# Kernel optimization log

Measured on AMD Instinct MI355X. Metric: run time of the kernel, lower is better.

The kernel has to match this reference:

```python
import jax, jax.numpy as jnp
import numpy as np

E = 1024   # embed_dim
H = 16     # num_heads
D = E // H # head_dim = 64
Q = 4      # num_queries
B = 4
S = 2048


def setup_inputs() -> dict:
    key = jax.random.key(0)
    ks = jax.random.split(key, 9)
    s = 0.02  # init scale for weights
    return {
        "x":  jax.random.normal(ks[0], (B, S, E), jnp.float32),
        "Wq": jax.random.normal(ks[1], (Q, E, E), jnp.float32) * s,  # stacked per-query Linear weights (torch layout: out,in)
        "bq": jax.random.normal(ks[2], (Q, E), jnp.float32) * s,
        "Wk": jax.random.normal(ks[3], (E, E), jnp.float32) * s,
        "bk": jax.random.normal(ks[4], (E,), jnp.float32) * s,
        "Wv": jax.random.normal(ks[5], (E, E), jnp.float32) * s,
        "bv": jax.random.normal(ks[6], (E,), jnp.float32) * s,
        "Wo": jax.random.normal(ks[7], (E, E), jnp.float32) * s,
        "bo": jax.random.normal(ks[8], (E,), jnp.float32) * s,
    }


def reference(x, Wq, bq, Wk, bk, Wv, bv, Wo, bo):
    B_, S_, E_ = x.shape
    scale = 1.0 / jnp.sqrt(jnp.asarray(D, x.dtype))
    # all query projections at once: (Q,B,S,E) -> (Q,B,S,H,D)
    q = (jnp.einsum('bse,qfe->qbsf', x, Wq) + bq[:, None, None, :]).reshape(Q, B_, S_, H, D)
    k = (x @ Wk.T + bk).reshape(B_, S_, H, D)
    v = (x @ Wv.T + bv).reshape(B_, S_, H, D)
    # NOTE: faithful to the torch code, which never moves the head axis before matmul:
    # scores[q,b,s,h,g] = sum_d q[q,b,s,h,d] * k[b,s,g,d]  -> softmax over heads g
    scores = jnp.einsum('qbshd,bsgd->qbshg', q, k) * scale      # (Q,B,S,H,H)
    probs = jax.nn.softmax(scores, axis=-1)
    out = jnp.einsum('qbshg,bsgd->qbshd', probs, v)             # (Q,B,S,H,D)
    # torch: .transpose(1,2).contiguous().view(B,S,E) == permute to (B,H,S,D) then reshape
    out = jnp.transpose(out, (0, 1, 3, 2, 4)).reshape(Q, B_, S_, E_)
    out = out.sum(axis=0)
    return out @ Wo.T + bo
```

## Files before the change

kernel.cpp:

```cpp
#include <hip/hip_runtime.h>


typedef __bf16 bf16x8 __attribute__((ext_vector_type(8)));
typedef float f32x4 __attribute__((ext_vector_type(4)));
typedef float f32x16 __attribute__((ext_vector_type(16)));

__device__ __forceinline__ unsigned short f2b(float f) {
  unsigned u = __float_as_uint(f);
  return (unsigned short)((u + 0x7fffu + ((u >> 16) & 1u)) >> 16);
}

__device__ __forceinline__ void async16(const void* g, void* l) {
  __builtin_amdgcn_global_load_lds(
      (const __attribute__((address_space(1))) void*)g,
      (__attribute__((address_space(3))) void*)l, 16, 0, 0);
}

__global__ __launch_bounds__(256) void cvt_all(
    const float* __restrict__ x, const float* __restrict__ Wq, const float* __restrict__ Wk,
    const float* __restrict__ Wv, const float* __restrict__ Wo, const float* __restrict__ bq,
    const float* __restrict__ bk, const float* __restrict__ bv,
    unsigned short* __restrict__ xb, unsigned short* __restrict__ wcat,
    unsigned short* __restrict__ wo_b, float* __restrict__ biascat) {
  if (blockIdx.x >= 15360) {
    int j = (blockIdx.x - 15360) * 256 + threadIdx.x;
    if (j < 6144) {
      float v = (j < 4096) ? bq[j] : (j < 5120 ? bk[j - 4096] : bv[j - 5120]);
      biascat[j] = v;
    }
    return;
  }
  int i = blockIdx.x * 256 + threadIdx.x;
  const float* s;
  unsigned short* d;
  int off;
  if (i < 2097152)      { s = x;  d = xb;             off = i; }
  else if (i < 3145728) { s = Wq; d = wcat;           off = i - 2097152; }
  else if (i < 3407872) { s = Wk; d = wcat + 4194304; off = i - 3145728; }
  else if (i < 3670016) { s = Wv; d = wcat + 5242880; off = i - 3407872; }
  else                  { s = Wo; d = wo_b;           off = i - 3670016; }
  float4 v = ((const float4*)s)[off];
  uint2 o;
  o.x = (unsigned)f2b(v.x) | ((unsigned)f2b(v.y) << 16);
  o.y = (unsigned)f2b(v.z) | ((unsigned)f2b(v.w) << 16);
  ((uint2*)d)[off] = o;
}

__global__ __launch_bounds__(512, 2) void gemm256(
    const unsigned short* __restrict__ A, const unsigned short* __restrict__ Bt,
    const float* __restrict__ bias, unsigned short* __restrict__ C,
    int M, int N, int K) {
  __shared__ __align__(16) unsigned short As[4][8192];
  __shared__ __align__(16) unsigned short Bs[4][8192];
  const int t = threadIdx.x;
  const int lane = t & 63, w = t >> 6;
  const int l31 = lane & 31, lhi = lane >> 5;
  const int wm = (w >> 2) * 128, wn = (w & 3) * 64;
  const int bm0 = blockIdx.y * 256, bn0 = blockIdx.x * 256;

  const int p0 = t & 7, pr0 = t >> 3;
  const int u0 = p0 ^ (pr0 & 7);
  const size_t aoff0 = (size_t)(2 * pr0 + (u0 & 1)) * K + (u0 >> 1) * 8;
  const unsigned short* aS0 = A + (size_t)bm0 * K + aoff0;
  const unsigned short* aS1 = aS0 + (size_t)128 * K;
  const unsigned short* bS0 = Bt + (size_t)bn0 * K + aoff0;
  const unsigned short* bS1 = bS0 + (size_t)128 * K;
  const int d0 = t * 8, d1 = d0 + 4096;

  const int plo = 2 * lhi + (l31 & 1);
  const int pswz = (l31 >> 1) & 7;
  const int pg0 = ((0 + plo) ^ pswz) * 8;
  const int pg1 = ((4 + plo) ^ pswz) * 8;
  int prA[4], prB[2];
#pragma unroll
  for (int mi = 0; mi < 4; ++mi) prA[mi] = ((wm + mi * 32 + l31) >> 1) * 64;
#pragma unroll
  for (int nj = 0; nj < 2; ++nj) prB[nj] = ((wn + nj * 32 + l31) >> 1) * 64;

  f32x16 acc[4][2];
#pragma unroll
  for (int mi = 0; mi < 4; ++mi)
#pragma unroll
    for (int nj = 0; nj < 2; ++nj)
#pragma unroll
      for (int e = 0; e < 16; ++e) acc[mi][nj][e] = 0.f;

#define STG_A(kt_) do { const int b_ = (kt_) & 3; const int ko_ = (kt_) * 32; \
    async16(aS0 + ko_, &As[b_][d0]); async16(aS1 + ko_, &As[b_][d1]); } while (0)
#define STG_B(kt_) do { const int b_ = (kt_) & 3; const int ko_ = (kt_) * 32; \
    async16(bS0 + ko_, &Bs[b_][d0]); async16(bS1 + ko_, &Bs[b_][d1]); } while (0)

  const int NT = K >> 5;
  STG_A(0); STG_B(0); STG_A(1); STG_B(1);
  asm volatile("s_waitcnt vmcnt(4)" ::: "memory");
  asm volatile("s_barrier" ::: "memory");

  for (int kt = 0; kt < NT; ++kt) {
    const int bi = kt & 3;
    const unsigned short* as_ = As[bi];
    const unsigned short* bs_ = Bs[bi];

    bf16x8 af[4][2], bfv[2][2];
#pragma unroll
    for (int mi = 0; mi < 4; ++mi) {
      af[mi][0] = *(const bf16x8*)(as_ + prA[mi] + pg0);
      af[mi][1] = *(const bf16x8*)(as_ + prA[mi] + pg1);
    }
#pragma unroll
    for (int nj = 0; nj < 2; ++nj) {
      bfv[nj][0] = *(const bf16x8*)(bs_ + prB[nj] + pg0);
      bfv[nj][1] = *(const bf16x8*)(bs_ + prB[nj] + pg1);
    }
    if (kt + 2 < NT) { STG_A(kt + 2); STG_B(kt + 2); }

#pragma unroll
    for (int mi = 0; mi < 4; ++mi)
#pragma unroll
      for (int nj = 0; nj < 2; ++nj) {
        acc[mi][nj] = __builtin_amdgcn_mfma_f32_32x32x16_bf16(af[mi][0], bfv[nj][0], acc[mi][nj], 0, 0, 0);
        acc[mi][nj] = __builtin_amdgcn_mfma_f32_32x32x16_bf16(af[mi][1], bfv[nj][1], acc[mi][nj], 0, 0, 0);
      }

    if (kt + 2 < NT) {
      asm volatile("s_waitcnt vmcnt(4)" ::: "memory");
    } else if (kt + 1 < NT) {
      asm volatile("s_waitcnt vmcnt(0)" ::: "memory");
    }
    asm volatile("s_barrier" ::: "memory");
  }
#undef STG_A
#undef STG_B

#pragma unroll
  for (int mi = 0; mi < 4; ++mi) {
#pragma unroll
    for (int nj = 0; nj < 2; ++nj) {
      int gc = bn0 + wn + nj * 32 + l31;
      float bsv = bias[gc];
#pragma unroll
      for (int reg = 0; reg < 16; ++reg) {
        int gr = bm0 + wm + mi * 32 + (reg & 3) + 8 * (reg >> 2) + 4 * lhi;
        C[(size_t)gr * N + gc] = f2b(acc[mi][nj][reg] + bsv);
      }
    }
  }
}

template <typename OutT>
__global__ __launch_bounds__(256) void gemm_bt(const unsigned short* __restrict__ A,
                                               const unsigned short* __restrict__ Bt,
                                               const float* __restrict__ bias,
                                               OutT* __restrict__ C, int M, int N, int K) {
  __shared__ __align__(16) unsigned short As[128 * 64];
  __shared__ __align__(16) unsigned short Bs[128 * 64];
  const int t = threadIdx.x;
  const int lane = t & 63, w = t >> 6;
  const int wm = (w >> 1) * 64, wn = (w & 1) * 64;
  const int l31 = lane & 31, lhi = lane >> 5;
  const int bm0 = blockIdx.y * 128, bn0 = blockIdx.x * 128;

  f32x16 acc[2][2];
#pragma unroll
  for (int i = 0; i < 2; ++i)
#pragma unroll
    for (int j = 0; j < 2; ++j)
#pragma unroll
      for (int e = 0; e < 16; ++e) acc[i][j][e] = 0.f;

  const int swz = l31 & 7;
  const int qoff = 2 * ((l31 >> 4) & 1);

  for (int k0 = 0; k0 < K; k0 += 64) {
    __syncthreads();
#pragma unroll
    for (int j = 0; j < 4; ++j) {
      int slot = j * 256 + t;
      int r = slot >> 3;
      int p = slot & 7;
      int c = (((p ^ (r & 7)) - 2 * ((r >> 4) & 1)) & 7) * 8;
      async16(A + (size_t)(bm0 + r) * K + k0 + c, As + slot * 8);
      async16(Bt + (size_t)(bn0 + r) * K + k0 + c, Bs + slot * 8);
    }
    __syncthreads();
#pragma unroll
    for (int kk = 0; kk < 64; kk += 16) {
      const int kg = kk >> 3;
      const int pg = ((((kg + lhi + qoff) & 7) ^ swz) << 3);
      bf16x8 af[2], bfr[2];
#pragma unroll
      for (int i = 0; i < 2; ++i)
        af[i] = *(const bf16x8*)(As + (wm + i * 32 + l31) * 64 + pg);
#pragma unroll
      for (int j = 0; j < 2; ++j)
        bfr[j] = *(const bf16x8*)(Bs + (wn + j * 32 + l31) * 64 + pg);
#pragma unroll
      for (int i = 0; i < 2; ++i)
#pragma unroll
        for (int j = 0; j < 2; ++j)
          acc[i][j] = __builtin_amdgcn_mfma_f32_32x32x16_bf16(af[i], bfr[j], acc[i][j], 0, 0, 0);
    }
  }

#pragma unroll
  for (int i = 0; i < 2; ++i) {
#pragma unroll
    for (int j = 0; j < 2; ++j) {
      int gc = bn0 + wn + j * 32 + l31;
      float bsv = bias[gc];
#pragma unroll
      for (int reg = 0; reg < 16; ++reg) {
        int gr = bm0 + wm + i * 32 + (reg & 3) + 8 * (reg >> 2) + 4 * lhi;
        float vv = acc[i][j][reg] + bsv;
        if constexpr (sizeof(OutT) == 2)
          C[(size_t)gr * N + gc] = (OutT)f2b(vv);
        else
          C[(size_t)gr * N + gc] = vv;
      }
    }
  }
}

__global__ __launch_bounds__(256) void attn_scatter(const unsigned short* __restrict__ qkv,
                                                    unsigned short* __restrict__ t) {
  __shared__ __align__(16) unsigned short vs[4][1024];
  __shared__ float ps[4][16 * 17];
  const int w = threadIdx.x >> 6, lane = threadIdx.x & 63;
  const int pos = blockIdx.x * 4 + w;
  const int b = pos >> 11, s = pos & 2047;
  const unsigned short* row = qkv + (size_t)pos * 6144;
  unsigned short* vw = vs[w];
  float* pw = ps[w];
  const int lr = lane & 15, lq = lane >> 4;

  {
    const uint4* sv = (const uint4*)(row + 5120);
    uint4* dv = (uint4*)vw;
    dv[lane * 2] = sv[lane * 2];
    dv[lane * 2 + 1] = sv[lane * 2 + 1];
  }
  bf16x8 kf0 = *(const bf16x8*)(row + 4096 + lr * 64 + lq * 8);
  bf16x8 kf1 = *(const bf16x8*)(row + 4096 + lr * 64 + 32 + lq * 8);

  bf16x8 vf[4];
#pragma unroll
  for (int dc = 0; dc < 4; ++dc) {
#pragma unroll
    for (int j = 0; j < 8; ++j) vf[dc][j] = (__bf16)0.0f;
    if (lq < 2) {
      const __bf16* vb = (const __bf16*)vw;
#pragma unroll
      for (int j = 0; j < 8; ++j)
        vf[dc][j] = vb[(lq * 8 + j) * 64 + dc * 16 + lr];
    }
  }

  f32x4 acc[4];
#pragma unroll
  for (int dc = 0; dc < 4; ++dc) acc[dc] = (f32x4){0.f, 0.f, 0.f, 0.f};

#pragma unroll
  for (int qi = 0; qi < 4; ++qi) {
    bf16x8 qf0 = *(const bf16x8*)(row + qi * 1024 + lr * 64 + lq * 8);
    bf16x8 qf1 = *(const bf16x8*)(row + qi * 1024 + lr * 64 + 32 + lq * 8);
    f32x4 sc = {0.f, 0.f, 0.f, 0.f};
    sc = __builtin_amdgcn_mfma_f32_16x16x32_bf16(qf0, kf0, sc, 0, 0, 0);
    sc = __builtin_amdgcn_mfma_f32_16x16x32_bf16(qf1, kf1, sc, 0, 0, 0);
#pragma unroll
    for (int r = 0; r < 4; ++r) {
      float e = __expf(sc[r] * 0.125f);
      float sum = e;
#pragma unroll
      for (int d = 1; d < 16; d <<= 1) sum += __shfl_xor(sum, d);
      pw[(lq * 4 + r) * 17 + lr] = e / sum;
    }
    bf16x8 pf;
#pragma unroll
    for (int j = 0; j < 8; ++j) pf[j] = (__bf16)0.0f;
    if (lq < 2) {
#pragma unroll
      for (int j = 0; j < 8; ++j) pf[j] = (__bf16)pw[lr * 17 + lq * 8 + j];
    }
#pragma unroll
    for (int dc = 0; dc < 4; ++dc)
      acc[dc] = __builtin_amdgcn_mfma_f32_16x16x32_bf16(vf[dc], pf, acc[dc], 0, 0, 0);
  }

  size_t base = ((size_t)(b * 2048 + 128 * lr + (s >> 4))) * 1024 + 64 * (s & 15) + lq * 4;
#pragma unroll
  for (int dc = 0; dc < 4; ++dc) {
    uint2 u;
    u.x = (unsigned)f2b(acc[dc][0]) | ((unsigned)f2b(acc[dc][1]) << 16);
    u.y = (unsigned)f2b(acc[dc][2]) | ((unsigned)f2b(acc[dc][3]) << 16);
    *(uint2*)(t + base + dc * 16) = u;
  }
}

extern "C" void kernel_launch(void* const* d_in, const int* in_sizes, int n_in,
                              void* d_out, int out_size, void* d_ws, size_t ws_size,
                              hipStream_t stream) {
  const float* x  = (const float*)d_in[0];
  const float* Wq = (const float*)d_in[1];
  const float* bq = (const float*)d_in[2];
  const float* Wk = (const float*)d_in[3];
  const float* bk = (const float*)d_in[4];
  const float* Wv = (const float*)d_in[5];
  const float* bv = (const float*)d_in[6];
  const float* Wo = (const float*)d_in[7];
  const float* bo = (const float*)d_in[8];
  float* out = (float*)d_out;

  char* ws = (char*)d_ws;
  unsigned short* xb      = (unsigned short*)(ws + 0);
  unsigned short* wcat    = (unsigned short*)(ws + 16777216);
  unsigned short* wo_b    = (unsigned short*)(ws + 29360128);
  float*          biascat = (float*)(ws + 31457280);
  unsigned short* qkv     = (unsigned short*)(ws + 31481856);
  unsigned short* t       = xb;

  cvt_all<<<15384, 256, 0, stream>>>(x, Wq, Wk, Wv, Wo, bq, bk, bv, xb, wcat, wo_b, biascat);

  gemm256<<<dim3(24, 32), 512, 0, stream>>>(xb, wcat, biascat, qkv, 8192, 6144, 1024);
  attn_scatter<<<2048, 256, 0, stream>>>(qkv, t);
  gemm_bt<float><<<dim3(8, 64), 256, 0, stream>>>(t, wo_b, bo, out, 8192, 1024, 1024);
}
```

Measured before the change: 277.7 us.

## Pipeline output-projection GEMM with 4-stage async LDS buffers; vectorize softmax staging

Replaces the single-buffered output GEMM with a kernel that uses four LDS stages of K=32 tiles, prefetches two tiles ahead via async global-to-LDS loads, and syncs with raw waitcnt/barrier instead of paired __syncthreads. It also requests two blocks per CU through launch bounds. In the attention kernel, the probability scratch is padded to 20 floats so it can be read back as float4 vectors, and the softmax division becomes a hardware reciprocal. The pipelined GEMM is meant to hide global-load latency behind MFMA work. In exchange it uses more LDS, its hand-written wait counts must match the number of outstanding loads exactly, and the reciprocal is slightly less precise.

```diff
diff --git a/kernel.cpp b/kernel.cpp
--- a/kernel.cpp
+++ b/kernel.cpp
@@ -146,75 +146,101 @@
   }
 }
 
-template <typename OutT>
-__global__ __launch_bounds__(256) void gemm_bt(const unsigned short* __restrict__ A,
-                                               const unsigned short* __restrict__ Bt,
-                                               const float* __restrict__ bias,
-                                               OutT* __restrict__ C, int M, int N, int K) {
-  __shared__ __align__(16) unsigned short As[128 * 64];
-  __shared__ __align__(16) unsigned short Bs[128 * 64];
+__global__ __launch_bounds__(256, 2) void gemm128(
+    const unsigned short* __restrict__ A, const unsigned short* __restrict__ Bt,
+    const float* __restrict__ bias, float* __restrict__ C,
+    int M, int N, int K) {
+  __shared__ __align__(16) unsigned short As[4][4096];
+  __shared__ __align__(16) unsigned short Bs[4][4096];
   const int t = threadIdx.x;
   const int lane = t & 63, w = t >> 6;
+  const int l31 = lane & 31, lhi = lane >> 5;
   const int wm = (w >> 1) * 64, wn = (w & 1) * 64;
-  const int l31 = lane & 31, lhi = lane >> 5;
   const int bm0 = blockIdx.y * 128, bn0 = blockIdx.x * 128;
 
+  const int p0 = t & 7, pr0 = t >> 3;
+  const int u0 = p0 ^ (pr0 & 7);
+  const size_t aoff0 = (size_t)(2 * pr0 + (u0 & 1)) * K + (u0 >> 1) * 8;
+  const unsigned short* aS0 = A + (size_t)bm0 * K + aoff0;
+  const unsigned short* aS1 = aS0 + (size_t)64 * K;
+  const unsigned short* bS0 = Bt + (size_t)bn0 * K + aoff0;
+  const unsigned short* bS1 = bS0 + (size_t)64 * K;
+  const int d0 = t * 8, d1 = d0 + 2048;
+
+  const int plo = 2 * lhi + (l31 & 1);
+  const int pswz = (l31 >> 1) & 7;
+  const int pg0 = ((0 + plo) ^ pswz) * 8;
+  const int pg1 = ((4 + plo) ^ pswz) * 8;
+  int prA[2], prB[2];
+#pragma unroll
+  for (int mi = 0; mi < 2; ++mi) prA[mi] = ((wm + mi * 32 + l31) >> 1) * 64;
+#pragma unroll
+  for (int nj = 0; nj < 2; ++nj) prB[nj] = ((wn + nj * 32 + l31) >> 1) * 64;
+
   f32x16 acc[2][2];
 #pragma unroll
-  for (int i = 0; i < 2; ++i)
-#pragma unroll
-    for (int j = 0; j < 2; ++j)
-#pragma unroll
-      for (int e = 0; e < 16; ++e) acc[i][j][e] = 0.f;
-
-  const int swz = l31 & 7;
-  const int qoff = 2 * ((l31 >> 4) & 1);
-
-  for (int k0 = 0; k0 < K; k0 += 64) {
-    __syncthreads();
-#pragma unroll
-    for (int j = 0; j < 4; ++j) {
-      int slot = j * 256 + t;
-      int r = slot >> 3;
-      int p = slot & 7;
-      int c = (((p ^ (r & 7)) - 2 * ((r >> 4) & 1)) & 7) * 8;
-      async16(A + (size_t)(bm0 + r) * K + k0 + c, As + slot * 8);
-      async16(Bt + (size_t)(bn0 + r) * K + k0 + c, Bs + slot * 8);
-    }
-    __syncthreads();
-#pragma unroll
-    for (int kk = 0; kk < 64; kk += 16) {
-      const int kg = kk >> 3;
-      const int pg = ((((kg + lhi + qoff) & 7) ^ swz) << 3);
-      bf16x8 af[2], bfr[2];
-#pragma unroll
-      for (int i = 0; i < 2; ++i)
-        af[i] = *(const bf16x8*)(As + (wm + i * 32 + l31) * 64 + pg);
-#pragma unroll
-      for (int j = 0; j < 2; ++j)
-        bfr[j] = *(const bf16x8*)(Bs + (wn + j * 32 + l31) * 64 + pg);
-#pragma unroll
-      for (int i = 0; i < 2; ++i)
-#pragma unroll
-        for (int j = 0; j < 2; ++j)
-          acc[i][j] = __builtin_amdgcn_mfma_f32_32x32x16_bf16(af[i], bfr[j], acc[i][j], 0, 0, 0);
-    }
-  }
-
-#pragma unroll
-  for (int i = 0; i < 2; ++i) {
-#pragma unroll
-    for (int j = 0; j < 2; ++j) {
-      int gc = bn0 + wn + j * 32 + l31;
+  for (int mi = 0; mi < 2; ++mi)
+#pragma unroll
+    for (int nj = 0; nj < 2; ++nj)
+#pragma unroll
+      for (int e = 0; e < 16; ++e) acc[mi][nj][e] = 0.f;
+
+#define STG_A(kt_) do { const int b_ = (kt_) & 3; const int ko_ = (kt_) * 32; \
+    async16(aS0 + ko_, &As[b_][d0]); async16(aS1 + ko_, &As[b_][d1]); } while (0)
+#define STG_B(kt_) do { const int b_ = (kt_) & 3; const int ko_ = (kt_) * 32; \
+    async16(bS0 + ko_, &Bs[b_][d0]); async16(bS1 + ko_, &Bs[b_][d1]); } while (0)
+
+  const int NT = K >> 5;
+  STG_A(0); STG_B(0); STG_A(1); STG_B(1);
+  asm volatile("s_waitcnt vmcnt(4)" ::: "memory");
+  asm volatile("s_barrier" ::: "memory");
+
+  for (int kt = 0; kt < NT; ++kt) {
+    const int bi = kt & 3;
+    const unsigned short* as_ = As[bi];
+    const unsigned short* bs_ = Bs[bi];
+
+    bf16x8 af[2][2], bfv[2][2];
+#pragma unroll
+    for (int mi = 0; mi < 2; ++mi) {
+      af[mi][0] = *(const bf16x8*)(as_ + prA[mi] + pg0);
+      af[mi][1] = *(const bf16x8*)(as_ + prA[mi] + pg1);
+    }
+#pragma unroll
+    for (int nj = 0; nj < 2; ++nj) {
+      bfv[nj][0] = *(const bf16x8*)(bs_ + prB[nj] + pg0);
+      bfv[nj][1] = *(const bf16x8*)(bs_ + prB[nj] + pg1);
+    }
+    if (kt + 2 < NT) { STG_A(kt + 2); STG_B(kt + 2); }
+
+#pragma unroll
+    for (int mi = 0; mi < 2; ++mi)
+#pragma unroll
+      for (int nj = 0; nj < 2; ++nj) {
+        acc[mi][nj] = __builtin_amdgcn_mfma_f32_32x32x16_bf16(af[mi][0], bfv[nj][0], acc[mi][nj], 0, 0, 0);
+        acc[mi][nj] = __builtin_amdgcn_mfma_f32_32x32x16_bf16(af[mi][1], bfv[nj][1], acc[mi][nj], 0, 0, 0);
+      }
+
+    if (kt + 2 < NT) {
+      asm volatile("s_waitcnt vmcnt(4)" ::: "memory");
+    } else if (kt + 1 < NT) {
+      asm volatile("s_waitcnt vmcnt(0)" ::: "memory");
+    }
+    asm volatile("s_barrier" ::: "memory");
+  }
+#undef STG_A
+#undef STG_B
+
+#pragma unroll
+  for (int mi = 0; mi < 2; ++mi) {
+#pragma unroll
+    for (int nj = 0; nj < 2; ++nj) {
+      int gc = bn0 + wn + nj * 32 + l31;
       float bsv = bias[gc];
 #pragma unroll
       for (int reg = 0; reg < 16; ++reg) {
-        int gr = bm0 + wm + i * 32 + (reg & 3) + 8 * (reg >> 2) + 4 * lhi;
-        float vv = acc[i][j][reg] + bsv;
-        if constexpr (sizeof(OutT) == 2)
-          C[(size_t)gr * N + gc] = (OutT)f2b(vv);
-        else
-          C[(size_t)gr * N + gc] = vv;
+        int gr = bm0 + wm + mi * 32 + (reg & 3) + 8 * (reg >> 2) + 4 * lhi;
+        C[(size_t)gr * N + gc] = acc[mi][nj][reg] + bsv;
       }
     }
   }
@@ -223,7 +249,7 @@
 __global__ __launch_bounds__(256) void attn_scatter(const unsigned short* __restrict__ qkv,
                                                     unsigned short* __restrict__ t) {
   __shared__ __align__(16) unsigned short vs[4][1024];
-  __shared__ float ps[4][16 * 17];
+  __shared__ __align__(16) float ps[4][16 * 20];
   const int w = threadIdx.x >> 6, lane = threadIdx.x & 63;
   const int pos = blockIdx.x * 4 + w;
   const int b = pos >> 11, s = pos & 2047;
@@ -271,14 +297,18 @@
       float sum = e;
 #pragma unroll
       for (int d = 1; d < 16; d <<= 1) sum += __shfl_xor(sum, d);
-      pw[(lq * 4 + r) * 17 + lr] = e / sum;
+      pw[(lq * 4 + r) * 20 + lr] = e * __builtin_amdgcn_rcpf(sum);
     }
     bf16x8 pf;
 #pragma unroll
     for (int j = 0; j < 8; ++j) pf[j] = (__bf16)0.0f;
     if (lq < 2) {
-#pragma unroll
-      for (int j = 0; j < 8; ++j) pf[j] = (__bf16)pw[lr * 17 + lq * 8 + j];
+      const float4* pp = (const float4*)(pw + lr * 20 + lq * 8);
+      float4 pa = pp[0], pb = pp[1];
+      pf[0] = (__bf16)pa.x; pf[1] = (__bf16)pa.y;
+      pf[2] = (__bf16)pa.z; pf[3] = (__bf16)pa.w;
+      pf[4] = (__bf16)pb.x; pf[5] = (__bf16)pb.y;
+      pf[6] = (__bf16)pb.z; pf[7] = (__bf16)pb.w;
     }
 #pragma unroll
     for (int dc = 0; dc < 4; ++dc)
@@ -321,5 +351,5 @@
 
   gemm256<<<dim3(24, 32), 512, 0, stream>>>(xb, wcat, biascat, qkv, 8192, 6144, 1024);
   attn_scatter<<<2048, 256, 0, stream>>>(qkv, t);
-  gemm_bt<float><<<dim3(8, 64), 256, 0, stream>>>(t, wo_b, bo, out, 8192, 1024, 1024);
-}
+  gemm128<<<dim3(8, 64), 256, 0, stream>>>(t, wo_b, bo, out, 8192, 1024, 1024);
+}
```

Result: no change. 278.6 us (+0.3%).
